# Performance work log

Measured on AMD Instinct MI355X. Metric: run time of the kernel, lower is better.

Reference implementation:

```python
import jax, jax.numpy as jnp
import numpy as np

N = 100000   # nodes
E = 1600000  # edges
IN = 128
H = 128
C = 2
EPS = 1e-5   # BatchNorm eps (torch default)


def setup_inputs() -> dict:
    key = jax.random.key(0)
    ks = jax.random.split(key, 40)
    d = {}
    d["x"] = jax.random.normal(ks[0], (N, IN), jnp.float32)
    d["edge_index"] = jax.random.randint(ks[1], (2, E), 0, N, dtype=jnp.int32)
    dims = [(IN, H), (H, H), (H, H), (H, H // 2), (H // 2, C)]
    for i, (a, b) in enumerate(dims):
        d[f"W{i+1}"] = jax.random.normal(ks[2 + 2 * i], (a, b), jnp.float32) / np.float32(np.sqrt(a))
        d[f"b{i+1}"] = jnp.zeros((b,), jnp.float32)
    bdims = [H, H, H, H // 2]
    for i, bd in enumerate(bdims):
        d[f"g{i+1}"] = 1.0 + 0.1 * jax.random.normal(ks[12 + 4 * i], (bd,), jnp.float32)
        d[f"be{i+1}"] = 0.1 * jax.random.normal(ks[13 + 4 * i], (bd,), jnp.float32)
        d[f"rm{i+1}"] = 0.1 * jax.random.normal(ks[14 + 4 * i], (bd,), jnp.float32)
        d[f"rv{i+1}"] = 1.0 + 0.1 * jax.random.uniform(ks[15 + 4 * i], (bd,), jnp.float32)
    return d


def _gcn_conv(x, W, b, src, dst, dinv):
    # PyG GCNConv: h = x @ W; symmetric-norm aggregation with self-loops; + bias
    h = x @ W                                            # [N, out]
    norm = dinv[src] * dinv[dst]                         # [E]
    msg = h[src] * norm[:, None]                         # gather + scale
    agg = jax.ops.segment_sum(msg, dst, num_segments=N)  # scatter-add at dst
    agg = agg + (dinv * dinv)[:, None] * h               # self-loop term
    return agg + b


def _bn_eval(h, g, be, rm, rv):
    # BatchNorm1d in eval mode (running stats)
    return (h - rm) * jax.lax.rsqrt(rv + EPS) * g + be


def reference(x, edge_index,
              W1, b1, W2, b2, W3, b3, W4, b4, W5, b5,
              g1, be1, rm1, rv1, g2, be2, rm2, rv2,
              g3, be3, rm3, rv3, g4, be4, rm4, rv4):
    src, dst = edge_index[0], edge_index[1]
    # degree with self-loops (edge weight 1), computed at destination nodes
    deg = jax.ops.segment_sum(jnp.ones((E,), x.dtype), dst, num_segments=N) + 1.0
    dinv = jax.lax.rsqrt(deg)

    h = jax.nn.relu(_bn_eval(_gcn_conv(x, W1, b1, src, dst, dinv), g1, be1, rm1, rv1))
    h = jax.nn.relu(_bn_eval(_gcn_conv(h, W2, b2, src, dst, dinv), g2, be2, rm2, rv2))
    h = jax.nn.relu(_bn_eval(_gcn_conv(h, W3, b3, src, dst, dinv), g3, be3, rm3, rv3))
    h = jax.nn.relu(_bn_eval(_gcn_conv(h, W4, b4, src, dst, dinv), g4, be4, rm4, rv4))
    return _gcn_conv(h, W5, b5, src, dst, dinv)  # [N, C]
```

## Files before the change

kernel.cpp:

```cpp
#include <hip/hip_runtime.h>
#include <hip/hip_fp16.h>

#define BN_EPS 1e-5f
#define CAP 8192
#define MAXBKT 512

typedef _Float16 half8 __attribute__((ext_vector_type(8)));
typedef float f32x4 __attribute__((ext_vector_type(4)));


__global__ void k_init(int* bucket_cur, int* rowptr, int n, int E) {
    int i = blockIdx.x * blockDim.x + threadIdx.x;
    if (i < MAXBKT) bucket_cur[i] = 0;
    if (i == 0) rowptr[n] = E;
}

__global__ __launch_bounds__(256) void k_bin(const int* __restrict__ src,
        const int* __restrict__ dst, int E, int nbk,
        int* __restrict__ bucket_cur, uint2* __restrict__ pairs) {
    __shared__ int hist[MAXBKT];
    __shared__ int base_[MAXBKT];
    for (int b = threadIdx.x; b < nbk; b += 256) hist[b] = 0;
    __syncthreads();
    int e0 = blockIdx.x * 2048;
    int my_b[8], my_l[8], my_s[8], my_d[8];
    #pragma unroll
    for (int j = 0; j < 8; j++) {
        int e = e0 + threadIdx.x + j * 256;
        my_b[j] = -1;
        if (e < E) {
            int d = dst[e];
            my_s[j] = src[e];
            my_d[j] = d;
            my_b[j] = d >> 8;
            my_l[j] = atomicAdd(&hist[my_b[j]], 1);
        }
    }
    __syncthreads();
    for (int b = threadIdx.x; b < nbk; b += 256) {
        int h = hist[b];
        base_[b] = h ? atomicAdd(&bucket_cur[b], h) : 0;
    }
    __syncthreads();
    #pragma unroll
    for (int j = 0; j < 8; j++) {
        if (my_b[j] >= 0) {
            int pos = base_[my_b[j]] + my_l[j];
            if (pos < CAP)
                pairs[(size_t)my_b[j] * CAP + pos] = make_uint2((unsigned)my_s[j], (unsigned)my_d[j]);
        }
    }
}

__global__ __launch_bounds__(256) void k_cnt(const uint2* __restrict__ pairs,
        const int* __restrict__ bucket_cur, int* __restrict__ cnt, int n) {
    __shared__ int lc[256];
    lc[threadIdx.x] = 0;
    __syncthreads();
    int b = blockIdx.x;
    int m = min(bucket_cur[b], CAP);
    const uint2* p = pairs + (size_t)b * CAP;
    for (int q = threadIdx.x; q < m; q += 256)
        atomicAdd(&lc[p[q].y & 255], 1);
    __syncthreads();
    int node = b * 256 + threadIdx.x;
    if (node < n) cnt[node] = lc[threadIdx.x];
}

__global__ void k_scan1(const int* __restrict__ cnt, int* __restrict__ rowptr,
                        int* __restrict__ bsums, int n) {
    __shared__ int tmp[256];
    int i = blockIdx.x * 256 + threadIdx.x;
    int v = (i < n) ? cnt[i] : 0;
    tmp[threadIdx.x] = v;
    __syncthreads();
    for (int off = 1; off < 256; off <<= 1) {
        int t = (threadIdx.x >= off) ? tmp[threadIdx.x - off] : 0;
        __syncthreads();
        tmp[threadIdx.x] += t;
        __syncthreads();
    }
    if (i < n) rowptr[i] = tmp[threadIdx.x] - v;
    if (threadIdx.x == 255) bsums[blockIdx.x] = tmp[255];
}

__global__ void k_scan2(int* bsums, int nb) {
    __shared__ int tmp[1024];
    int v = (threadIdx.x < nb) ? bsums[threadIdx.x] : 0;
    tmp[threadIdx.x] = v;
    __syncthreads();
    for (int off = 1; off < 1024; off <<= 1) {
        int t = (threadIdx.x >= off) ? tmp[threadIdx.x - off] : 0;
        __syncthreads();
        tmp[threadIdx.x] += t;
        __syncthreads();
    }
    if (threadIdx.x < nb) bsums[threadIdx.x] = tmp[threadIdx.x] - v;
}

__global__ void k_scan3(int* __restrict__ rowptr, const int* __restrict__ bsums,
                        const int* __restrict__ cnt, float* __restrict__ dinv, int n) {
    int i = blockIdx.x * blockDim.x + threadIdx.x;
    if (i < n) {
        rowptr[i] += bsums[i >> 8];
        dinv[i] = rsqrtf((float)cnt[i] + 1.0f);
    }
}

__global__ __launch_bounds__(256) void k_fill2(const uint2* __restrict__ pairs,
        const int* __restrict__ bucket_cur, const int* __restrict__ rowptr,
        int* __restrict__ csr, int n) {
    __shared__ int cur[256];
    __shared__ int stg[CAP];
    int b = blockIdx.x;
    int node0 = b * 256;
    int nend = min(node0 + 256, n);
    int base_csr = rowptr[node0];
    int node = node0 + threadIdx.x;
    cur[threadIdx.x] = (node < n) ? rowptr[node] - base_csr : 0;
    __syncthreads();
    int m = min(bucket_cur[b], CAP);
    const uint2* p = pairs + (size_t)b * CAP;
    for (int q = threadIdx.x; q < m; q += 256) {
        uint2 pr = p[q];
        int ofs = atomicAdd(&cur[pr.y & 255], 1);
        stg[ofs] = (int)pr.x;
    }
    __syncthreads();
    int len = rowptr[nend] - base_csr;
    for (int q = threadIdx.x; q < len; q += 256)
        csr[base_csr + q] = stg[q];
}


template<int M>
__global__ void k_wpack(const float* __restrict__ W, half8* __restrict__ Wp) {
    int idx = blockIdx.x * 256 + threadIdx.x;
    constexpr int TOT = (M / 16) * 4 * 64;
    if (idx >= TOT) return;
    int l = idx & 63, tc = idx >> 6;
    int c = tc & 3, t = tc >> 2;
    int g = l >> 4, nn = l & 15;
    int k0 = 32 * c + 8 * g, col = 16 * t + nn;
    half8 hi, lo;
    #pragma unroll
    for (int j = 0; j < 8; j++) {
        float w = W[(size_t)(k0 + j) * M + col];
        _Float16 h = (_Float16)w;
        hi[j] = h;
        lo[j] = (_Float16)(w - (float)h);
    }
    Wp[idx] = hi;
    Wp[TOT + idx] = lo;
}


template<int M, bool A_FP32>
__global__ __launch_bounds__(256) void k_gemm_mfma(const void* __restrict__ Ain,
        const half8* __restrict__ Wp, const float* __restrict__ dinv,
        __half* __restrict__ out, int n) {
    constexpr int NT = M / 16;
    constexpr int TPW = NT / 4;
    constexpr int LDR = 136;
    __shared__ _Float16 As[64 * LDR];

    int row0 = blockIdx.x * 64;
    for (int idx = threadIdx.x; idx < 64 * 16; idx += 256) {
        int r = idx >> 4, k2 = idx & 15;
        int grow = row0 + r;
        half8 h = {};
        if (grow < n) {
            if constexpr (A_FP32) {
                const float* Af = (const float*)Ain;
                float4 va = *(const float4*)&Af[(size_t)grow * 128 + k2 * 8];
                float4 vb = *(const float4*)&Af[(size_t)grow * 128 + k2 * 8 + 4];
                h[0] = (_Float16)va.x; h[1] = (_Float16)va.y;
                h[2] = (_Float16)va.z; h[3] = (_Float16)va.w;
                h[4] = (_Float16)vb.x; h[5] = (_Float16)vb.y;
                h[6] = (_Float16)vb.z; h[7] = (_Float16)vb.w;
            } else {
                h = *(const half8*)((const __half*)Ain + (size_t)grow * 128 + k2 * 8);
            }
        }
        *(half8*)&As[r * LDR + k2 * 8] = h;
    }
    __syncthreads();

    int w = threadIdx.x >> 6, l = threadIdx.x & 63;
    int g = l >> 4, nn = l & 15;

    half8 xf[4][4];
    #pragma unroll
    for (int rg = 0; rg < 4; rg++)
        #pragma unroll
        for (int c = 0; c < 4; c++)
            xf[rg][c] = *(const half8*)&As[(16 * rg + nn) * LDR + (4 * c + g) * 8];

    f32x4 acc[4][TPW];
    #pragma unroll
    for (int rg = 0; rg < 4; rg++)
        #pragma unroll
        for (int tt = 0; tt < TPW; tt++)
            acc[rg][tt] = (f32x4){0.f, 0.f, 0.f, 0.f};

    #pragma unroll
    for (int tt = 0; tt < TPW; tt++) {
        int t = w * TPW + tt;
        #pragma unroll
        for (int c = 0; c < 4; c++) {
            half8 wh = Wp[(t * 4 + c) * 64 + l];
            half8 wl = Wp[NT * 4 * 64 + (t * 4 + c) * 64 + l];
            #pragma unroll
            for (int rg = 0; rg < 4; rg++) {
                acc[rg][tt] = __builtin_amdgcn_mfma_f32_16x16x32_f16(wh, xf[rg][c], acc[rg][tt], 0, 0, 0);
                acc[rg][tt] = __builtin_amdgcn_mfma_f32_16x16x32_f16(wl, xf[rg][c], acc[rg][tt], 0, 0, 0);
            }
        }
    }

    __syncthreads();
    #pragma unroll
    for (int rg = 0; rg < 4; rg++) {
        int node = row0 + 16 * rg + nn;
        float s = (node < n) ? dinv[node] : 0.f;
        #pragma unroll
        for (int tt = 0; tt < TPW; tt++) {
            int colh = 16 * (w * TPW + tt) + 4 * g;
            __half2 p0 = __float22half2_rn(make_float2(acc[rg][tt][0] * s, acc[rg][tt][1] * s));
            __half2 p1 = __float22half2_rn(make_float2(acc[rg][tt][2] * s, acc[rg][tt][3] * s));
            uint2 u;
            u.x = *(unsigned*)&p0;
            u.y = *(unsigned*)&p1;
            *(uint2*)&As[(16 * rg + nn) * LDR + colh] = u;
        }
    }
    __syncthreads();
    for (int idx = threadIdx.x; idx < 64 * (M / 8); idx += 256) {
        int r = idx / (M / 8), k2 = idx % (M / 8);
        int grow = row0 + r;
        if (grow < n)
            *(uint4*)&out[(size_t)grow * M + k2 * 8] = *(const uint4*)&As[r * LDR + k2 * 8];
    }
}


__global__ void k_gemm5h(const __half* __restrict__ A, const float* __restrict__ W,
                         const float* __restrict__ dinv, float* __restrict__ out, int n) {
    __shared__ float Wl[128];
    if (threadIdx.x < 128) Wl[threadIdx.x] = W[threadIdx.x];
    __syncthreads();
    int i = blockIdx.x * blockDim.x + threadIdx.x;
    if (i >= n) return;
    float a0 = 0.f, a1 = 0.f;
    const __half2* Ar = (const __half2*)(A + (size_t)i * 64);
    #pragma unroll
    for (int k2 = 0; k2 < 32; k2++) {
        float2 x = __half22float2(Ar[k2]);
        a0 = fmaf(x.x, Wl[4 * k2 + 0], a0); a1 = fmaf(x.x, Wl[4 * k2 + 1], a1);
        a0 = fmaf(x.y, Wl[4 * k2 + 2], a0); a1 = fmaf(x.y, Wl[4 * k2 + 3], a1);
    }
    float s = dinv[i];
    out[2 * i] = a0 * s;
    out[2 * i + 1] = a1 * s;
}


__device__ __forceinline__ void h8_acc(float* acc, uint4 v) {
    const __half2* p = (const __half2*)&v;
    #pragma unroll
    for (int j = 0; j < 4; j++) {
        float2 f = __half22float2(p[j]);
        acc[2 * j] += f.x;
        acc[2 * j + 1] += f.y;
    }
}

template<int M16, bool BN>
__global__ __launch_bounds__(256) void k_agg_h(const __half* __restrict__ ht,
        const int* __restrict__ rowptr, const int* __restrict__ csr,
        const float* __restrict__ dinv, const float* __restrict__ bias,
        const float* __restrict__ gw, const float* __restrict__ bb,
        const float* __restrict__ rm, const float* __restrict__ rv,
        __half* __restrict__ out, int n) {
    constexpr int NPB = 256 / M16;
    constexpr int M = M16 * 8;
    int grp = threadIdx.x / M16;
    int c = threadIdx.x % M16;
    int i = blockIdx.x * NPB + grp;
    if (i >= n) return;
    const uint4* h4 = (const uint4*)ht;
    float acc[8] = {};
    h8_acc(acc, h4[(size_t)i * M16 + c]);
    int e1 = rowptr[i + 1];
    int e = rowptr[i];
    for (; e + 4 <= e1; e += 4) {
        int s0 = csr[e], s1 = csr[e + 1], s2 = csr[e + 2], s3 = csr[e + 3];
        uint4 v0 = h4[(size_t)s0 * M16 + c];
        uint4 v1 = h4[(size_t)s1 * M16 + c];
        uint4 v2 = h4[(size_t)s2 * M16 + c];
        uint4 v3 = h4[(size_t)s3 * M16 + c];
        h8_acc(acc, v0); h8_acc(acc, v1); h8_acc(acc, v2); h8_acc(acc, v3);
    }
    for (; e < e1; e++)
        h8_acc(acc, h4[(size_t)csr[e] * M16 + c]);

    float di = dinv[i];
    int c0 = c * 8;
    float4 b0 = *(const float4*)&bias[c0], b1 = *(const float4*)&bias[c0 + 4];
    float o[8];
    o[0] = fmaf(acc[0], di, b0.x); o[1] = fmaf(acc[1], di, b0.y);
    o[2] = fmaf(acc[2], di, b0.z); o[3] = fmaf(acc[3], di, b0.w);
    o[4] = fmaf(acc[4], di, b1.x); o[5] = fmaf(acc[5], di, b1.y);
    o[6] = fmaf(acc[6], di, b1.z); o[7] = fmaf(acc[7], di, b1.w);
    if (BN) {
        float gv[8], bbv[8], rmv[8], rvv[8];
        *(float4*)&gv[0] = *(const float4*)&gw[c0];  *(float4*)&gv[4] = *(const float4*)&gw[c0 + 4];
        *(float4*)&bbv[0] = *(const float4*)&bb[c0]; *(float4*)&bbv[4] = *(const float4*)&bb[c0 + 4];
        *(float4*)&rmv[0] = *(const float4*)&rm[c0]; *(float4*)&rmv[4] = *(const float4*)&rm[c0 + 4];
        *(float4*)&rvv[0] = *(const float4*)&rv[c0]; *(float4*)&rvv[4] = *(const float4*)&rv[c0 + 4];
        #pragma unroll
        for (int j = 0; j < 8; j++)
            o[j] = fmaxf(fmaf(o[j] - rmv[j], rsqrtf(rvv[j] + BN_EPS) * gv[j], bbv[j]), 0.f);
    }
    __half2 q0 = __float22half2_rn(make_float2(o[0], o[1]));
    __half2 q1 = __float22half2_rn(make_float2(o[2], o[3]));
    __half2 q2 = __float22half2_rn(make_float2(o[4], o[5]));
    __half2 q3 = __float22half2_rn(make_float2(o[6], o[7]));
    uint4 u;
    u.x = *(unsigned*)&q0; u.y = *(unsigned*)&q1;
    u.z = *(unsigned*)&q2; u.w = *(unsigned*)&q3;
    *(uint4*)&out[(size_t)i * M + c0] = u;
}

__global__ void k_agg_final(const float* __restrict__ ht, const int* __restrict__ rowptr,
                            const int* __restrict__ csr, const float* __restrict__ dinv,
                            const float* __restrict__ bias, float* __restrict__ out, int n) {
    int i = blockIdx.x * blockDim.x + threadIdx.x;
    if (i >= n) return;
    const float2* h2 = (const float2*)ht;
    float2 t = h2[i];
    float a0 = t.x, a1 = t.y;
    int e1 = rowptr[i + 1];
    int e = rowptr[i];
    for (; e + 4 <= e1; e += 4) {
        int s0 = csr[e], s1 = csr[e + 1], s2 = csr[e + 2], s3 = csr[e + 3];
        float2 u0 = h2[s0], u1 = h2[s1], u2 = h2[s2], u3 = h2[s3];
        a0 += (u0.x + u1.x) + (u2.x + u3.x);
        a1 += (u0.y + u1.y) + (u2.y + u3.y);
    }
    for (; e < e1; e++) {
        float2 u = h2[csr[e]];
        a0 += u.x; a1 += u.y;
    }
    float s = dinv[i];
    out[2 * i]     = fmaf(a0, s, bias[0]);
    out[2 * i + 1] = fmaf(a1, s, bias[1]);
}


extern "C" void kernel_launch(void* const* d_in, const int* in_sizes, int n_in,
                              void* d_out, int out_size, void* d_ws, size_t ws_size,
                              hipStream_t stream) {
    const float* x  = (const float*)d_in[0];
    const int*   ei = (const int*)d_in[1];
    const float* W1 = (const float*)d_in[2];  const float* b1 = (const float*)d_in[3];
    const float* W2 = (const float*)d_in[4];  const float* b2 = (const float*)d_in[5];
    const float* W3 = (const float*)d_in[6];  const float* b3 = (const float*)d_in[7];
    const float* W4 = (const float*)d_in[8];  const float* b4 = (const float*)d_in[9];
    const float* W5 = (const float*)d_in[10]; const float* b5 = (const float*)d_in[11];
    const float* g1 = (const float*)d_in[12]; const float* be1 = (const float*)d_in[13];
    const float* rm1 = (const float*)d_in[14]; const float* rv1 = (const float*)d_in[15];
    const float* g2 = (const float*)d_in[16]; const float* be2 = (const float*)d_in[17];
    const float* rm2 = (const float*)d_in[18]; const float* rv2 = (const float*)d_in[19];
    const float* g3 = (const float*)d_in[20]; const float* be3 = (const float*)d_in[21];
    const float* rm3 = (const float*)d_in[22]; const float* rv3 = (const float*)d_in[23];
    const float* g4 = (const float*)d_in[24]; const float* be4 = (const float*)d_in[25];
    const float* rm4 = (const float*)d_in[26]; const float* rv4 = (const float*)d_in[27];

    const int N = in_sizes[0] / 128;
    const int E = in_sizes[1] / 2;
    const int* src = ei;
    const int* dst = ei + E;
    const int nbk = (N + 255) >> 8;

    char* base = (char*)d_ws;
    size_t off = 0;
    auto carve = [&](size_t bytes) -> void* {
        void* r = base + off;
        off = (off + bytes + 255) & ~(size_t)255;
        return r;
    };
    __half* bufB16 = (__half*)carve((size_t)N * 128 * 2);
    __half* ht16   = (__half*)carve((size_t)N * 128 * 2);
    float*  htS    = (float*)carve((size_t)N * 2 * 4);
    half8*  Wp1 = (half8*)carve(2 * 8 * 4 * 64 * 16);
    half8*  Wp2 = (half8*)carve(2 * 8 * 4 * 64 * 16);
    half8*  Wp3 = (half8*)carve(2 * 8 * 4 * 64 * 16);
    half8*  Wp4 = (half8*)carve(2 * 4 * 4 * 64 * 16);
    uint2* pairs = (uint2*)carve((size_t)MAXBKT * CAP * 8);
    int*   bucket_cur = (int*)carve((size_t)MAXBKT * 4);
    int*   cnt   = (int*)carve((size_t)N * 4);
    int*   rowptr= (int*)carve((size_t)(N + 1) * 4);
    int*   csr   = (int*)carve((size_t)E * 4);
    float* dinv  = (float*)carve((size_t)N * 4);
    int*   bsums = (int*)carve((size_t)nbk * 4);
    (void)ws_size; (void)n_in; (void)out_size;

    float* out = (float*)d_out;

    k_wpack<128><<<8, 256, 0, stream>>>(W1, Wp1);
    k_wpack<128><<<8, 256, 0, stream>>>(W2, Wp2);
    k_wpack<128><<<8, 256, 0, stream>>>(W3, Wp3);
    k_wpack<64><<<4, 256, 0, stream>>>(W4, Wp4);

    k_init <<<(N + 255) / 256, 256, 0, stream>>>(bucket_cur, rowptr, N, E);
    k_bin  <<<(E + 2047) / 2048, 256, 0, stream>>>(src, dst, E, nbk, bucket_cur, pairs);
    k_cnt  <<<nbk, 256, 0, stream>>>(pairs, bucket_cur, cnt, N);
    k_scan1<<<nbk, 256, 0, stream>>>(cnt, rowptr, bsums, N);
    k_scan2<<<1, 1024, 0, stream>>>(bsums, nbk);
    k_scan3<<<(N + 255) / 256, 256, 0, stream>>>(rowptr, bsums, cnt, dinv, N);
    k_fill2<<<nbk, 256, 0, stream>>>(pairs, bucket_cur, rowptr, csr, N);

    const int gb = (N + 63) / 64;
    k_gemm_mfma<128, true><<<gb, 256, 0, stream>>>(x, Wp1, dinv, ht16, N);
    k_agg_h<16, true><<<(N + 15) / 16, 256, 0, stream>>>(ht16, rowptr, csr, dinv, b1, g1, be1, rm1, rv1, bufB16, N);
    k_gemm_mfma<128, false><<<gb, 256, 0, stream>>>(bufB16, Wp2, dinv, ht16, N);
    k_agg_h<16, true><<<(N + 15) / 16, 256, 0, stream>>>(ht16, rowptr, csr, dinv, b2, g2, be2, rm2, rv2, bufB16, N);
    k_gemm_mfma<128, false><<<gb, 256, 0, stream>>>(bufB16, Wp3, dinv, ht16, N);
    k_agg_h<16, true><<<(N + 15) / 16, 256, 0, stream>>>(ht16, rowptr, csr, dinv, b3, g3, be3, rm3, rv3, bufB16, N);
    k_gemm_mfma<64, false><<<gb, 256, 0, stream>>>(bufB16, Wp4, dinv, ht16, N);
    k_agg_h<8, true><<<(N + 31) / 32, 256, 0, stream>>>(ht16, rowptr, csr, dinv, b4, g4, be4, rm4, rv4, bufB16, N);
    k_gemm5h<<<(N + 255) / 256, 256, 0, stream>>>(bufB16, W5, dinv, htS, N);
    k_agg_final<<<(N + 255) / 256, 256, 0, stream>>>(htS, rowptr, csr, dinv, b5, out, N);
}
```

Baseline: 366.1 us.

## Fuse aggregation+BN+ReLU into next layer's MFMA GEMM and pack edge pairs

Each layer's neighbor aggregation, bias, BatchNorm and ReLU now run in the same kernel as the following MFMA GEMM. The aggregated rows go into shared memory instead of a global intermediate buffer, which removes a write and a read of the N×128 half-precision activations per layer. The final layer's small GEMM is fused the same way. Edge pairs are packed into one 32-bit word (24-bit src plus the low 8 bits of dst), halving the binning traffic, and the count and local scan kernels are merged, which also drops the cnt buffer. The packing assumes node ids fit in 24 bits, and the fused kernels do their gather with 64 rows per block, which may change the latency hiding and occupancy of the gather phase.

```diff
diff --git a/kernel.cpp b/kernel.cpp
--- a/kernel.cpp
+++ b/kernel.cpp
@@ -17,21 +17,21 @@
 
 __global__ __launch_bounds__(256) void k_bin(const int* __restrict__ src,
         const int* __restrict__ dst, int E, int nbk,
-        int* __restrict__ bucket_cur, uint2* __restrict__ pairs) {
+        int* __restrict__ bucket_cur, unsigned* __restrict__ pairs) {
     __shared__ int hist[MAXBKT];
     __shared__ int base_[MAXBKT];
     for (int b = threadIdx.x; b < nbk; b += 256) hist[b] = 0;
     __syncthreads();
     int e0 = blockIdx.x * 2048;
-    int my_b[8], my_l[8], my_s[8], my_d[8];
+    int my_b[8], my_l[8];
+    unsigned my_p[8];
     #pragma unroll
     for (int j = 0; j < 8; j++) {
         int e = e0 + threadIdx.x + j * 256;
         my_b[j] = -1;
         if (e < E) {
             int d = dst[e];
-            my_s[j] = src[e];
-            my_d[j] = d;
+            my_p[j] = (unsigned)src[e] | ((unsigned)(d & 255) << 24);
             my_b[j] = d >> 8;
             my_l[j] = atomicAdd(&hist[my_b[j]], 1);
         }
@@ -47,31 +47,25 @@
         if (my_b[j] >= 0) {
             int pos = base_[my_b[j]] + my_l[j];
             if (pos < CAP)
-                pairs[(size_t)my_b[j] * CAP + pos] = make_uint2((unsigned)my_s[j], (unsigned)my_d[j]);
-        }
-    }
-}
-
-__global__ __launch_bounds__(256) void k_cnt(const uint2* __restrict__ pairs,
-        const int* __restrict__ bucket_cur, int* __restrict__ cnt, int n) {
+                pairs[(size_t)my_b[j] * CAP + pos] = my_p[j];
+        }
+    }
+}
+
+__global__ __launch_bounds__(256) void k_cntscan(const unsigned* __restrict__ pairs,
+        const int* __restrict__ bucket_cur, int* __restrict__ rowptr,
+        int* __restrict__ bsums, float* __restrict__ dinv, int n) {
     __shared__ int lc[256];
+    __shared__ int tmp[256];
     lc[threadIdx.x] = 0;
     __syncthreads();
     int b = blockIdx.x;
     int m = min(bucket_cur[b], CAP);
-    const uint2* p = pairs + (size_t)b * CAP;
+    const unsigned* p = pairs + (size_t)b * CAP;
     for (int q = threadIdx.x; q < m; q += 256)
-        atomicAdd(&lc[p[q].y & 255], 1);
-    __syncthreads();
-    int node = b * 256 + threadIdx.x;
-    if (node < n) cnt[node] = lc[threadIdx.x];
-}
-
-__global__ void k_scan1(const int* __restrict__ cnt, int* __restrict__ rowptr,
-                        int* __restrict__ bsums, int n) {
-    __shared__ int tmp[256];
-    int i = blockIdx.x * 256 + threadIdx.x;
-    int v = (i < n) ? cnt[i] : 0;
+        atomicAdd(&lc[p[q] >> 24], 1);
+    __syncthreads();
+    int v = lc[threadIdx.x];
     tmp[threadIdx.x] = v;
     __syncthreads();
     for (int off = 1; off < 256; off <<= 1) {
@@ -80,8 +74,12 @@
         tmp[threadIdx.x] += t;
         __syncthreads();
     }
-    if (i < n) rowptr[i] = tmp[threadIdx.x] - v;
-    if (threadIdx.x == 255) bsums[blockIdx.x] = tmp[255];
+    int node = b * 256 + threadIdx.x;
+    if (node < n) {
+        rowptr[node] = tmp[threadIdx.x] - v;
+        dinv[node] = rsqrtf((float)v + 1.0f);
+    }
+    if (threadIdx.x == 255) bsums[b] = tmp[255];
 }
 
 __global__ void k_scan2(int* bsums, int nb) {
@@ -98,16 +96,12 @@
     if (threadIdx.x < nb) bsums[threadIdx.x] = tmp[threadIdx.x] - v;
 }
 
-__global__ void k_scan3(int* __restrict__ rowptr, const int* __restrict__ bsums,
-                        const int* __restrict__ cnt, float* __restrict__ dinv, int n) {
+__global__ void k_scan3(int* __restrict__ rowptr, const int* __restrict__ bsums, int n) {
     int i = blockIdx.x * blockDim.x + threadIdx.x;
-    if (i < n) {
-        rowptr[i] += bsums[i >> 8];
-        dinv[i] = rsqrtf((float)cnt[i] + 1.0f);
-    }
-}
-
-__global__ __launch_bounds__(256) void k_fill2(const uint2* __restrict__ pairs,
+    if (i < n) rowptr[i] += bsums[i >> 8];
+}
+
+__global__ __launch_bounds__(256) void k_fill2(const unsigned* __restrict__ pairs,
         const int* __restrict__ bucket_cur, const int* __restrict__ rowptr,
         int* __restrict__ csr, int n) {
     __shared__ int cur[256];
@@ -120,11 +114,11 @@
     cur[threadIdx.x] = (node < n) ? rowptr[node] - base_csr : 0;
     __syncthreads();
     int m = min(bucket_cur[b], CAP);
-    const uint2* p = pairs + (size_t)b * CAP;
+    const unsigned* p = pairs + (size_t)b * CAP;
     for (int q = threadIdx.x; q < m; q += 256) {
-        uint2 pr = p[q];
-        int ofs = atomicAdd(&cur[pr.y & 255], 1);
-        stg[ofs] = (int)pr.x;
+        unsigned pr = p[q];
+        int ofs = atomicAdd(&cur[pr >> 24], 1);
+        stg[ofs] = (int)(pr & 0xFFFFFFu);
     }
     __syncthreads();
     int len = rowptr[nend] - base_csr;
@@ -155,12 +149,20 @@
 }
 
 
-template<int M, bool A_FP32>
-__global__ __launch_bounds__(256) void k_gemm_mfma(const void* __restrict__ Ain,
+__device__ __forceinline__ void h8_acc(float* acc, uint4 v) {
+    const __half2* p = (const __half2*)&v;
+    #pragma unroll
+    for (int j = 0; j < 4; j++) {
+        float2 f = __half22float2(p[j]);
+        acc[2 * j] += f.x;
+        acc[2 * j + 1] += f.y;
+    }
+}
+
+
+__global__ __launch_bounds__(256) void k_gemm_mfma1(const float* __restrict__ Ain,
         const half8* __restrict__ Wp, const float* __restrict__ dinv,
         __half* __restrict__ out, int n) {
-    constexpr int NT = M / 16;
-    constexpr int TPW = NT / 4;
     constexpr int LDR = 136;
     __shared__ _Float16 As[64 * LDR];
 
@@ -170,17 +172,12 @@
         int grow = row0 + r;
         half8 h = {};
         if (grow < n) {
-            if constexpr (A_FP32) {
-                const float* Af = (const float*)Ain;
-                float4 va = *(const float4*)&Af[(size_t)grow * 128 + k2 * 8];
-                float4 vb = *(const float4*)&Af[(size_t)grow * 128 + k2 * 8 + 4];
-                h[0] = (_Float16)va.x; h[1] = (_Float16)va.y;
-                h[2] = (_Float16)va.z; h[3] = (_Float16)va.w;
-                h[4] = (_Float16)vb.x; h[5] = (_Float16)vb.y;
-                h[6] = (_Float16)vb.z; h[7] = (_Float16)vb.w;
-            } else {
-                h = *(const half8*)((const __half*)Ain + (size_t)grow * 128 + k2 * 8);
-            }
+            float4 va = *(const float4*)&Ain[(size_t)grow * 128 + k2 * 8];
+            float4 vb = *(const float4*)&Ain[(size_t)grow * 128 + k2 * 8 + 4];
+            h[0] = (_Float16)va.x; h[1] = (_Float16)va.y;
+            h[2] = (_Float16)va.z; h[3] = (_Float16)va.w;
+            h[4] = (_Float16)vb.x; h[5] = (_Float16)vb.y;
+            h[6] = (_Float16)vb.z; h[7] = (_Float16)vb.w;
         }
         *(half8*)&As[r * LDR + k2 * 8] = h;
     }
@@ -196,20 +193,20 @@
         for (int c = 0; c < 4; c++)
             xf[rg][c] = *(const half8*)&As[(16 * rg + nn) * LDR + (4 * c + g) * 8];
 
-    f32x4 acc[4][TPW];
+    f32x4 acc[4][2];
     #pragma unroll
     for (int rg = 0; rg < 4; rg++)
         #pragma unroll
-        for (int tt = 0; tt < TPW; tt++)
+        for (int tt = 0; tt < 2; tt++)
             acc[rg][tt] = (f32x4){0.f, 0.f, 0.f, 0.f};
 
     #pragma unroll
-    for (int tt = 0; tt < TPW; tt++) {
-        int t = w * TPW + tt;
+    for (int tt = 0; tt < 2; tt++) {
+        int t = w * 2 + tt;
         #pragma unroll
         for (int c = 0; c < 4; c++) {
             half8 wh = Wp[(t * 4 + c) * 64 + l];
-            half8 wl = Wp[NT * 4 * 64 + (t * 4 + c) * 64 + l];
+            half8 wl = Wp[8 * 4 * 64 + (t * 4 + c) * 64 + l];
             #pragma unroll
             for (int rg = 0; rg < 4; rg++) {
                 acc[rg][tt] = __builtin_amdgcn_mfma_f32_16x16x32_f16(wh, xf[rg][c], acc[rg][tt], 0, 0, 0);
@@ -224,8 +221,8 @@
         int node = row0 + 16 * rg + nn;
         float s = (node < n) ? dinv[node] : 0.f;
         #pragma unroll
-        for (int tt = 0; tt < TPW; tt++) {
-            int colh = 16 * (w * TPW + tt) + 4 * g;
+        for (int tt = 0; tt < 2; tt++) {
+            int colh = 16 * (w * 2 + tt) + 4 * g;
             __half2 p0 = __float22half2_rn(make_float2(acc[rg][tt][0] * s, acc[rg][tt][1] * s));
             __half2 p1 = __float22half2_rn(make_float2(acc[rg][tt][2] * s, acc[rg][tt][3] * s));
             uint2 u;
@@ -235,102 +232,215 @@
         }
     }
     __syncthreads();
-    for (int idx = threadIdx.x; idx < 64 * (M / 8); idx += 256) {
-        int r = idx / (M / 8), k2 = idx % (M / 8);
+    for (int idx = threadIdx.x; idx < 64 * 16; idx += 256) {
+        int r = idx >> 4, k2 = idx & 15;
         int grow = row0 + r;
         if (grow < n)
-            *(uint4*)&out[(size_t)grow * M + k2 * 8] = *(const uint4*)&As[r * LDR + k2 * 8];
-    }
-}
-
-
-__global__ void k_gemm5h(const __half* __restrict__ A, const float* __restrict__ W,
-                         const float* __restrict__ dinv, float* __restrict__ out, int n) {
-    __shared__ float Wl[128];
-    if (threadIdx.x < 128) Wl[threadIdx.x] = W[threadIdx.x];
-    __syncthreads();
-    int i = blockIdx.x * blockDim.x + threadIdx.x;
-    if (i >= n) return;
-    float a0 = 0.f, a1 = 0.f;
-    const __half2* Ar = (const __half2*)(A + (size_t)i * 64);
-    #pragma unroll
-    for (int k2 = 0; k2 < 32; k2++) {
-        float2 x = __half22float2(Ar[k2]);
-        a0 = fmaf(x.x, Wl[4 * k2 + 0], a0); a1 = fmaf(x.x, Wl[4 * k2 + 1], a1);
-        a0 = fmaf(x.y, Wl[4 * k2 + 2], a0); a1 = fmaf(x.y, Wl[4 * k2 + 3], a1);
-    }
-    float s = dinv[i];
-    out[2 * i] = a0 * s;
-    out[2 * i + 1] = a1 * s;
-}
-
-
-__device__ __forceinline__ void h8_acc(float* acc, uint4 v) {
-    const __half2* p = (const __half2*)&v;
-    #pragma unroll
-    for (int j = 0; j < 4; j++) {
-        float2 f = __half22float2(p[j]);
-        acc[2 * j] += f.x;
-        acc[2 * j + 1] += f.y;
-    }
-}
-
-template<int M16, bool BN>
-__global__ __launch_bounds__(256) void k_agg_h(const __half* __restrict__ ht,
+            *(uint4*)&out[(size_t)grow * 128 + k2 * 8] = *(const uint4*)&As[r * LDR + k2 * 8];
+    }
+}
+
+
+template<int MOUT>
+__global__ __launch_bounds__(256) void k_fused_mfma(const __half* __restrict__ ht,
         const int* __restrict__ rowptr, const int* __restrict__ csr,
         const float* __restrict__ dinv, const float* __restrict__ bias,
         const float* __restrict__ gw, const float* __restrict__ bb,
         const float* __restrict__ rm, const float* __restrict__ rv,
-        __half* __restrict__ out, int n) {
-    constexpr int NPB = 256 / M16;
-    constexpr int M = M16 * 8;
-    int grp = threadIdx.x / M16;
-    int c = threadIdx.x % M16;
-    int i = blockIdx.x * NPB + grp;
-    if (i >= n) return;
+        const half8* __restrict__ Wp, __half* __restrict__ out, int n) {
+    constexpr int NT = MOUT / 16;
+    constexpr int TPW = NT / 4;
+    constexpr int LDR = 136;
+    __shared__ _Float16 As[64 * LDR];
+
+    int row0 = blockIdx.x * 64;
+    int grp = threadIdx.x >> 4;
+    int c = threadIdx.x & 15;
     const uint4* h4 = (const uint4*)ht;
-    float acc[8] = {};
-    h8_acc(acc, h4[(size_t)i * M16 + c]);
-    int e1 = rowptr[i + 1];
-    int e = rowptr[i];
-    for (; e + 4 <= e1; e += 4) {
-        int s0 = csr[e], s1 = csr[e + 1], s2 = csr[e + 2], s3 = csr[e + 3];
-        uint4 v0 = h4[(size_t)s0 * M16 + c];
-        uint4 v1 = h4[(size_t)s1 * M16 + c];
-        uint4 v2 = h4[(size_t)s2 * M16 + c];
-        uint4 v3 = h4[(size_t)s3 * M16 + c];
-        h8_acc(acc, v0); h8_acc(acc, v1); h8_acc(acc, v2); h8_acc(acc, v3);
-    }
-    for (; e < e1; e++)
-        h8_acc(acc, h4[(size_t)csr[e] * M16 + c]);
-
-    float di = dinv[i];
     int c0 = c * 8;
-    float4 b0 = *(const float4*)&bias[c0], b1 = *(const float4*)&bias[c0 + 4];
-    float o[8];
-    o[0] = fmaf(acc[0], di, b0.x); o[1] = fmaf(acc[1], di, b0.y);
-    o[2] = fmaf(acc[2], di, b0.z); o[3] = fmaf(acc[3], di, b0.w);
-    o[4] = fmaf(acc[4], di, b1.x); o[5] = fmaf(acc[5], di, b1.y);
-    o[6] = fmaf(acc[6], di, b1.z); o[7] = fmaf(acc[7], di, b1.w);
-    if (BN) {
-        float gv[8], bbv[8], rmv[8], rvv[8];
-        *(float4*)&gv[0] = *(const float4*)&gw[c0];  *(float4*)&gv[4] = *(const float4*)&gw[c0 + 4];
-        *(float4*)&bbv[0] = *(const float4*)&bb[c0]; *(float4*)&bbv[4] = *(const float4*)&bb[c0 + 4];
-        *(float4*)&rmv[0] = *(const float4*)&rm[c0]; *(float4*)&rmv[4] = *(const float4*)&rm[c0 + 4];
-        *(float4*)&rvv[0] = *(const float4*)&rv[c0]; *(float4*)&rvv[4] = *(const float4*)&rv[c0 + 4];
-        #pragma unroll
-        for (int j = 0; j < 8; j++)
-            o[j] = fmaxf(fmaf(o[j] - rmv[j], rsqrtf(rvv[j] + BN_EPS) * gv[j], bbv[j]), 0.f);
-    }
-    __half2 q0 = __float22half2_rn(make_float2(o[0], o[1]));
-    __half2 q1 = __float22half2_rn(make_float2(o[2], o[3]));
-    __half2 q2 = __float22half2_rn(make_float2(o[4], o[5]));
-    __half2 q3 = __float22half2_rn(make_float2(o[6], o[7]));
-    uint4 u;
-    u.x = *(unsigned*)&q0; u.y = *(unsigned*)&q1;
-    u.z = *(unsigned*)&q2; u.w = *(unsigned*)&q3;
-    *(uint4*)&out[(size_t)i * M + c0] = u;
-}
+    float4 bv0 = *(const float4*)&bias[c0], bv1 = *(const float4*)&bias[c0 + 4];
+    float gv[8], bbv[8], rmv[8], rvv[8];
+    *(float4*)&gv[0] = *(const float4*)&gw[c0];  *(float4*)&gv[4] = *(const float4*)&gw[c0 + 4];
+    *(float4*)&bbv[0] = *(const float4*)&bb[c0]; *(float4*)&bbv[4] = *(const float4*)&bb[c0 + 4];
+    *(float4*)&rmv[0] = *(const float4*)&rm[c0]; *(float4*)&rmv[4] = *(const float4*)&rm[c0 + 4];
+    *(float4*)&rvv[0] = *(const float4*)&rv[c0]; *(float4*)&rvv[4] = *(const float4*)&rv[c0 + 4];
+
+    for (int p = 0; p < 4; p++) {
+        int r = p * 16 + grp;
+        int i = row0 + r;
+        uint4 u = make_uint4(0, 0, 0, 0);
+        if (i < n) {
+            float acc[8] = {};
+            h8_acc(acc, h4[(size_t)i * 16 + c]);
+            int e1 = rowptr[i + 1];
+            int e = rowptr[i];
+            for (; e + 4 <= e1; e += 4) {
+                int s0 = csr[e], s1 = csr[e + 1], s2 = csr[e + 2], s3 = csr[e + 3];
+                uint4 v0 = h4[(size_t)s0 * 16 + c];
+                uint4 v1 = h4[(size_t)s1 * 16 + c];
+                uint4 v2 = h4[(size_t)s2 * 16 + c];
+                uint4 v3 = h4[(size_t)s3 * 16 + c];
+                h8_acc(acc, v0); h8_acc(acc, v1); h8_acc(acc, v2); h8_acc(acc, v3);
+            }
+            for (; e < e1; e++)
+                h8_acc(acc, h4[(size_t)csr[e] * 16 + c]);
+            float di = dinv[i];
+            float o[8];
+            o[0] = fmaf(acc[0], di, bv0.x); o[1] = fmaf(acc[1], di, bv0.y);
+            o[2] = fmaf(acc[2], di, bv0.z); o[3] = fmaf(acc[3], di, bv0.w);
+            o[4] = fmaf(acc[4], di, bv1.x); o[5] = fmaf(acc[5], di, bv1.y);
+            o[6] = fmaf(acc[6], di, bv1.z); o[7] = fmaf(acc[7], di, bv1.w);
+            #pragma unroll
+            for (int j = 0; j < 8; j++)
+                o[j] = fmaxf(fmaf(o[j] - rmv[j], rsqrtf(rvv[j] + BN_EPS) * gv[j], bbv[j]), 0.f);
+            __half2 q0 = __float22half2_rn(make_float2(o[0], o[1]));
+            __half2 q1 = __float22half2_rn(make_float2(o[2], o[3]));
+            __half2 q2 = __float22half2_rn(make_float2(o[4], o[5]));
+            __half2 q3 = __float22half2_rn(make_float2(o[6], o[7]));
+            u.x = *(unsigned*)&q0; u.y = *(unsigned*)&q1;
+            u.z = *(unsigned*)&q2; u.w = *(unsigned*)&q3;
+        }
+        *(uint4*)&As[r * LDR + c0] = u;
+    }
+    __syncthreads();
+
+    int w = threadIdx.x >> 6, l = threadIdx.x & 63;
+    int g = l >> 4, nn = l & 15;
+
+    half8 xf[4][4];
+    #pragma unroll
+    for (int rg = 0; rg < 4; rg++)
+        #pragma unroll
+        for (int cc = 0; cc < 4; cc++)
+            xf[rg][cc] = *(const half8*)&As[(16 * rg + nn) * LDR + (4 * cc + g) * 8];
+
+    f32x4 acc2[4][TPW];
+    #pragma unroll
+    for (int rg = 0; rg < 4; rg++)
+        #pragma unroll
+        for (int tt = 0; tt < TPW; tt++)
+            acc2[rg][tt] = (f32x4){0.f, 0.f, 0.f, 0.f};
+
+    #pragma unroll
+    for (int tt = 0; tt < TPW; tt++) {
+        int t = w * TPW + tt;
+        #pragma unroll
+        for (int cc = 0; cc < 4; cc++) {
+            half8 wh = Wp[(t * 4 + cc) * 64 + l];
+            half8 wl = Wp[NT * 4 * 64 + (t * 4 + cc) * 64 + l];
+            #pragma unroll
+            for (int rg = 0; rg < 4; rg++) {
+                acc2[rg][tt] = __builtin_amdgcn_mfma_f32_16x16x32_f16(wh, xf[rg][cc], acc2[rg][tt], 0, 0, 0);
+                acc2[rg][tt] = __builtin_amdgcn_mfma_f32_16x16x32_f16(wl, xf[rg][cc], acc2[rg][tt], 0, 0, 0);
+            }
+        }
+    }
+
+    __syncthreads();
+    #pragma unroll
+    for (int rg = 0; rg < 4; rg++) {
+        int node = row0 + 16 * rg + nn;
+        float s = (node < n) ? dinv[node] : 0.f;
+        #pragma unroll
+        for (int tt = 0; tt < TPW; tt++) {
+            int colh = 16 * (w * TPW + tt) + 4 * g;
+            __half2 p0 = __float22half2_rn(make_float2(acc2[rg][tt][0] * s, acc2[rg][tt][1] * s));
+            __half2 p1 = __float22half2_rn(make_float2(acc2[rg][tt][2] * s, acc2[rg][tt][3] * s));
+            uint2 uu;
+            uu.x = *(unsigned*)&p0;
+            uu.y = *(unsigned*)&p1;
+            *(uint2*)&As[(16 * rg + nn) * LDR + colh] = uu;
+        }
+    }
+    __syncthreads();
+    for (int idx = threadIdx.x; idx < 64 * (MOUT / 8); idx += 256) {
+        int r = idx / (MOUT / 8), k2 = idx % (MOUT / 8);
+        int grow = row0 + r;
+        if (grow < n)
+            *(uint4*)&out[(size_t)grow * MOUT + k2 * 8] = *(const uint4*)&As[r * LDR + k2 * 8];
+    }
+}
+
+
+__global__ __launch_bounds__(256) void k_fused5(const __half* __restrict__ ht,
+        const int* __restrict__ rowptr, const int* __restrict__ csr,
+        const float* __restrict__ dinv, const float* __restrict__ bias,
+        const float* __restrict__ gw, const float* __restrict__ bb,
+        const float* __restrict__ rm, const float* __restrict__ rv,
+        const float* __restrict__ W5, float* __restrict__ outS, int n) {
+    constexpr int LDR = 72;
+    __shared__ _Float16 As[64 * LDR];
+    __shared__ float Wl[128];
+    if (threadIdx.x < 128) Wl[threadIdx.x] = W5[threadIdx.x];
+
+    int row0 = blockIdx.x * 64;
+    int grp = threadIdx.x >> 3;
+    int c = threadIdx.x & 7;
+    const uint4* h4 = (const uint4*)ht;
+    int c0 = c * 8;
+    float4 bv0 = *(const float4*)&bias[c0], bv1 = *(const float4*)&bias[c0 + 4];
+    float gv[8], bbv[8], rmv[8], rvv[8];
+    *(float4*)&gv[0] = *(const float4*)&gw[c0];  *(float4*)&gv[4] = *(const float4*)&gw[c0 + 4];
+    *(float4*)&bbv[0] = *(const float4*)&bb[c0]; *(float4*)&bbv[4] = *(const float4*)&bb[c0 + 4];
+    *(float4*)&rmv[0] = *(const float4*)&rm[c0]; *(float4*)&rmv[4] = *(const float4*)&rm[c0 + 4];
+    *(float4*)&rvv[0] = *(const float4*)&rv[c0]; *(float4*)&rvv[4] = *(const float4*)&rv[c0 + 4];
+
+    for (int p = 0; p < 2; p++) {
+        int r = p * 32 + grp;
+        int i = row0 + r;
+        uint4 u = make_uint4(0, 0, 0, 0);
+        if (i < n) {
+            float acc[8] = {};
+            h8_acc(acc, h4[(size_t)i * 8 + c]);
+            int e1 = rowptr[i + 1];
+            int e = rowptr[i];
+            for (; e + 4 <= e1; e += 4) {
+                int s0 = csr[e], s1 = csr[e + 1], s2 = csr[e + 2], s3 = csr[e + 3];
+                uint4 v0 = h4[(size_t)s0 * 8 + c];
+                uint4 v1 = h4[(size_t)s1 * 8 + c];
+                uint4 v2 = h4[(size_t)s2 * 8 + c];
+                uint4 v3 = h4[(size_t)s3 * 8 + c];
+                h8_acc(acc, v0); h8_acc(acc, v1); h8_acc(acc, v2); h8_acc(acc, v3);
+            }
+            for (; e < e1; e++)
+                h8_acc(acc, h4[(size_t)csr[e] * 8 + c]);
+            float di = dinv[i];
+            float o[8];
+            o[0] = fmaf(acc[0], di, bv0.x); o[1] = fmaf(acc[1], di, bv0.y);
+            o[2] = fmaf(acc[2], di, bv0.z); o[3] = fmaf(acc[3], di, bv0.w);
+            o[4] = fmaf(acc[4], di, bv1.x); o[5] = fmaf(acc[5], di, bv1.y);
+            o[6] = fmaf(acc[6], di, bv1.z); o[7] = fmaf(acc[7], di, bv1.w);
+            #pragma unroll
+            for (int j = 0; j < 8; j++)
+                o[j] = fmaxf(fmaf(o[j] - rmv[j], rsqrtf(rvv[j] + BN_EPS) * gv[j], bbv[j]), 0.f);
+            __half2 q0 = __float22half2_rn(make_float2(o[0], o[1]));
+            __half2 q1 = __float22half2_rn(make_float2(o[2], o[3]));
+            __half2 q2 = __float22half2_rn(make_float2(o[4], o[5]));
+            __half2 q3 = __float22half2_rn(make_float2(o[6], o[7]));
+            u.x = *(unsigned*)&q0; u.y = *(unsigned*)&q1;
+            u.z = *(unsigned*)&q2; u.w = *(unsigned*)&q3;
+        }
+        *(uint4*)&As[r * LDR + c0] = u;
+    }
+    __syncthreads();
+
+    if (threadIdx.x < 128) {
+        int r = threadIdx.x >> 1, cls = threadIdx.x & 1;
+        int i = row0 + r;
+        if (i < n) {
+            float a = 0.f;
+            const __half2* row = (const __half2*)&As[r * LDR];
+            #pragma unroll
+            for (int k2 = 0; k2 < 32; k2++) {
+                float2 xx = __half22float2(row[k2]);
+                a = fmaf(xx.x, Wl[4 * k2 + cls], a);
+                a = fmaf(xx.y, Wl[4 * k2 + 2 + cls], a);
+            }
+            outS[2 * i + cls] = a * dinv[i];
+        }
+    }
+}
+
 
 __global__ void k_agg_final(const float* __restrict__ ht, const int* __restrict__ rowptr,
                             const int* __restrict__ csr, const float* __restrict__ dinv,
@@ -390,16 +500,15 @@
         off = (off + bytes + 255) & ~(size_t)255;
         return r;
     };
-    __half* bufB16 = (__half*)carve((size_t)N * 128 * 2);
-    __half* ht16   = (__half*)carve((size_t)N * 128 * 2);
-    float*  htS    = (float*)carve((size_t)N * 2 * 4);
+    __half* htA = (__half*)carve((size_t)N * 128 * 2);
+    __half* htB = (__half*)carve((size_t)N * 128 * 2);
+    float*  htS = (float*)carve((size_t)N * 2 * 4);
     half8*  Wp1 = (half8*)carve(2 * 8 * 4 * 64 * 16);
     half8*  Wp2 = (half8*)carve(2 * 8 * 4 * 64 * 16);
     half8*  Wp3 = (half8*)carve(2 * 8 * 4 * 64 * 16);
     half8*  Wp4 = (half8*)carve(2 * 4 * 4 * 64 * 16);
-    uint2* pairs = (uint2*)carve((size_t)MAXBKT * CAP * 8);
+    unsigned* pairs = (unsigned*)carve((size_t)MAXBKT * CAP * 4);
     int*   bucket_cur = (int*)carve((size_t)MAXBKT * 4);
-    int*   cnt   = (int*)carve((size_t)N * 4);
     int*   rowptr= (int*)carve((size_t)(N + 1) * 4);
     int*   csr   = (int*)carve((size_t)E * 4);
     float* dinv  = (float*)carve((size_t)N * 4);
@@ -413,23 +522,18 @@
     k_wpack<128><<<8, 256, 0, stream>>>(W3, Wp3);
     k_wpack<64><<<4, 256, 0, stream>>>(W4, Wp4);
 
-    k_init <<<(N + 255) / 256, 256, 0, stream>>>(bucket_cur, rowptr, N, E);
-    k_bin  <<<(E + 2047) / 2048, 256, 0, stream>>>(src, dst, E, nbk, bucket_cur, pairs);
-    k_cnt  <<<nbk, 256, 0, stream>>>(pairs, bucket_cur, cnt, N);
-    k_scan1<<<nbk, 256, 0, stream>>>(cnt, rowptr, bsums, N);
-    k_scan2<<<1, 1024, 0, stream>>>(bsums, nbk);
-    k_scan3<<<(N + 255) / 256, 256, 0, stream>>>(rowptr, bsums, cnt, dinv, N);
-    k_fill2<<<nbk, 256, 0, stream>>>(pairs, bucket_cur, rowptr, csr, N);
+    k_init   <<<(N + 255) / 256, 256, 0, stream>>>(bucket_cur, rowptr, N, E);
+    k_bin    <<<(E + 2047) / 2048, 256, 0, stream>>>(src, dst, E, nbk, bucket_cur, pairs);
+    k_cntscan<<<nbk, 256, 0, stream>>>(pairs, bucket_cur, rowptr, bsums, dinv, N);
+    k_scan2  <<<1, 1024, 0, stream>>>(bsums, nbk);
+    k_scan3  <<<(N + 255) / 256, 256, 0, stream>>>(rowptr, bsums, N);
+    k_fill2  <<<nbk, 256, 0, stream>>>(pairs, bucket_cur, rowptr, csr, N);
 
     const int gb = (N + 63) / 64;
-    k_gemm_mfma<128, true><<<gb, 256, 0, stream>>>(x, Wp1, dinv, ht16, N);
-    k_agg_h<16, true><<<(N + 15) / 16, 256, 0, stream>>>(ht16, rowptr, csr, dinv, b1, g1, be1, rm1, rv1, bufB16, N);
-    k_gemm_mfma<128, false><<<gb, 256, 0, stream>>>(bufB16, Wp2, dinv, ht16, N);
-    k_agg_h<16, true><<<(N + 15) / 16, 256, 0, stream>>>(ht16, rowptr, csr, dinv, b2, g2, be2, rm2, rv2, bufB16, N);
-    k_gemm_mfma<128, false><<<gb, 256, 0, stream>>>(bufB16, Wp3, dinv, ht16, N);
-    k_agg_h<16, true><<<(N + 15) / 16, 256, 0, stream>>>(ht16, rowptr, csr, dinv, b3, g3, be3, rm3, rv3, bufB16, N);
-    k_gemm_mfma<64, false><<<gb, 256, 0, stream>>>(bufB16, Wp4, dinv, ht16, N);
-    k_agg_h<8, true><<<(N + 31) / 32, 256, 0, stream>>>(ht16, rowptr, csr, dinv, b4, g4, be4, rm4, rv4, bufB16, N);
-    k_gemm5h<<<(N + 255) / 256, 256, 0, stream>>>(bufB16, W5, dinv, htS, N);
+    k_gemm_mfma1<<<gb, 256, 0, stream>>>(x, Wp1, dinv, htA, N);
+    k_fused_mfma<128><<<gb, 256, 0, stream>>>(htA, rowptr, csr, dinv, b1, g1, be1, rm1, rv1, Wp2, htB, N);
+    k_fused_mfma<128><<<gb, 256, 0, stream>>>(htB, rowptr, csr, dinv, b2, g2, be2, rm2, rv2, Wp3, htA, N);
+    k_fused_mfma<64><<<gb, 256, 0, stream>>>(htA, rowptr, csr, dinv, b3, g3, be3, rm3, rv3, Wp4, htB, N);
+    k_fused5<<<gb, 256, 0, stream>>>(htB, rowptr, csr, dinv, b4, g4, be4, rm4, rv4, W5, htS, N);
     k_agg_final<<<(N + 255) / 256, 256, 0, stream>>>(htS, rowptr, csr, dinv, b5, out, N);
 }
```

Measured after the change: 359.7 us. About the same (-1.7%).
